# Kernel optimization log

Hardware: AMD Instinct MI355X
Metric: run time of the kernel (lower is better)

## Reference

```python
import jax, jax.numpy as jnp
import numpy as np

D_MODEL = 1024
NUM_HEAD = 16
D_HEAD = D_MODEL // NUM_HEAD
LN_EPS = 1e-5


def setup_inputs() -> dict:
    key = jax.random.key(0)
    ks = jax.random.split(key, 4)
    B, S = 4, 2048
    x = jax.random.normal(ks[0], (B, S, D_MODEL), dtype=jnp.float32)
    Wq = jax.random.normal(ks[1], (D_MODEL, D_MODEL), dtype=jnp.float32) * 0.02
    Wk = jax.random.normal(ks[2], (D_MODEL, D_MODEL), dtype=jnp.float32) * 0.02
    Wv = jax.random.normal(ks[3], (D_MODEL, D_MODEL), dtype=jnp.float32) * 0.02
    return {
        "x": x,
        "Wq": Wq, "bq": jnp.zeros((D_MODEL,), jnp.float32),
        "Wk": Wk, "bk": jnp.zeros((D_MODEL,), jnp.float32),
        "Wv": Wv, "bv": jnp.zeros((D_MODEL,), jnp.float32),
        "gamma": jnp.ones((D_MODEL,), jnp.float32),
        "beta": jnp.zeros((D_MODEL,), jnp.float32),
    }


def _layer_norm(x, gamma, beta):
    mu = jnp.mean(x, axis=-1, keepdims=True)
    var = jnp.mean(jnp.square(x - mu), axis=-1, keepdims=True)
    return (x - mu) * jax.lax.rsqrt(var + LN_EPS) * gamma + beta


def reference(x, Wq, bq, Wk, bk, Wv, bv, gamma, beta):
    # x: (B, S, D). Prefill path (kv_cache=None); dropout is eval-mode identity.
    B, S, D = x.shape
    q = (x @ Wq + bq).reshape(B, S, NUM_HEAD, D_HEAD).transpose(0, 2, 1, 3)  # (B,H,S,dh)
    k = (x @ Wk + bk).reshape(B, S, NUM_HEAD, D_HEAD).transpose(0, 2, 1, 3)
    v = (x @ Wv + bv).reshape(B, S, NUM_HEAD, D_HEAD).transpose(0, 2, 1, 3)
    scores = jnp.einsum("bhqd,bhkd->bhqk", q, k) / jnp.sqrt(jnp.float32(D_HEAD))
    causal = jnp.tril(jnp.ones((S, S), dtype=bool))  # (S, Skv) with no cache
    scores = jnp.where(causal[None, None], scores, -jnp.inf)
    w = jax.nn.softmax(scores, axis=-1)
    attn = jnp.einsum("bhqk,bhkd->bhqd", w, v).transpose(0, 2, 1, 3).reshape(B, S, D)
    out = _layer_norm(x + attn, gamma, beta)
    return out, k, v  # (output, new K cache, new V cache)
```

## Files before the change

kernel.cpp:

```cpp
#include <hip/hip_runtime.h>
#include <math.h>

#define D_MODEL 1024
#define NUM_HEAD 16
#define D_HEAD   64
#define BATCH    4
#define SEQ      2048
#define MTOT     (BATCH*SEQ)

typedef __attribute__((ext_vector_type(8))) short short8;
typedef __attribute__((ext_vector_type(4))) short short4v;
typedef __attribute__((ext_vector_type(2))) short short2v;
typedef __attribute__((ext_vector_type(4))) float f32x4;

static __device__ __forceinline__ unsigned short f2bf_u(float f) {
    union { float f; unsigned u; } v; v.f = f;
    return (unsigned short)((v.u + 0x7FFFu + ((v.u >> 16) & 1u)) >> 16);
}
static __device__ __forceinline__ short f2bf(float f) { return (short)f2bf_u(f); }
static __device__ __forceinline__ float bf2f(unsigned short h) {
    union { float f; unsigned u; } v; v.u = ((unsigned)h) << 16; return v.f;
}

#define ASYNC16(ldst, gsrc) __builtin_amdgcn_global_load_lds( \
    (const __attribute__((address_space(1))) unsigned int*)(gsrc), \
    (__attribute__((address_space(3))) unsigned int*)(ldst), 16, 0, 0)

__global__ __launch_bounds__(256) void conv_x(
    const float* __restrict__ x, unsigned short* __restrict__ hi,
    unsigned short* __restrict__ lo, int m0)
{
    const int gid = blockIdx.x * 256 + threadIdx.x;
    const int ml = gid >> 7;
    const int k  = (gid & 127) << 3;
    const float* s = &x[(size_t)(m0 + ml) * D_MODEL + k];
    float4 a = *(const float4*)s;
    float4 b = *(const float4*)(s + 4);
    float vv[8] = {a.x, a.y, a.z, a.w, b.x, b.y, b.z, b.w};
    short8 ph, pl;
#pragma unroll
    for (int j = 0; j < 8; ++j) {
        unsigned short h = f2bf_u(vv[j]);
        ph[j] = (short)h;
        pl[j] = (short)f2bf_u(vv[j] - bf2f(h));
    }
    size_t off = ((size_t)(ml >> 7) * 32 + (k >> 5)) * 4096
               + (size_t)(ml & 127) * 32 + (k & 31);
    *(short8*)&hi[off] = ph;
    *(short8*)&lo[off] = pl;
}

__global__ __launch_bounds__(256) void conv_w(
    const float* __restrict__ W, unsigned short* __restrict__ hi,
    unsigned short* __restrict__ lo)
{
    __shared__ float Tr[32][132];
    const int t  = threadIdx.x;
    const int n0 = blockIdx.x * 128, k0 = blockIdx.y * 32;
#pragma unroll
    for (int it = 0; it < 4; ++it) {
        int idx = it * 256 + t;
        int kr = idx >> 5, c = (idx & 31) * 4;
        *(float4*)&Tr[kr][c] = *(const float4*)&W[(size_t)(k0 + kr) * D_MODEL + n0 + c];
    }
    __syncthreads();
    const int n = t >> 1, kh = (t & 1) * 16;
    short8 ph0, ph1, pl0, pl1;
#pragma unroll
    for (int j = 0; j < 16; ++j) {
        float v = Tr[kh + j][n];
        unsigned short h = f2bf_u(v);
        unsigned short lw = f2bf_u(v - bf2f(h));
        if (j < 8) { ph0[j] = (short)h; pl0[j] = (short)lw; }
        else       { ph1[j - 8] = (short)h; pl1[j - 8] = (short)lw; }
    }
    size_t base = ((size_t)blockIdx.x * 32 + blockIdx.y) * 4096 + (size_t)n * 32 + kh;
    *(short8*)&hi[base]     = ph0;
    *(short8*)&hi[base + 8] = ph1;
    *(short8*)&lo[base]     = pl0;
    *(short8*)&lo[base + 8] = pl1;
}

__global__ __launch_bounds__(256) void gemm3(
    const unsigned short* __restrict__ Ah, const unsigned short* __restrict__ Al,
    const unsigned short* __restrict__ Bh, const unsigned short* __restrict__ Bl,
    const float* __restrict__ bias, float* __restrict__ Y, int m0)
{
    __shared__ unsigned short lds[16384];
    unsigned short* LA  = lds;
    unsigned short* LB  = lds + 4096;
    unsigned short* LAl = lds + 8192;
    unsigned short* LBl = lds + 12288;

    const int t  = threadIdx.x;
    const int l  = t & 63, w = t >> 6;
    const int lq = l & 15, g = l >> 4;
    const int wr = w >> 1, wc = w & 1;

    const size_t abase = (size_t)blockIdx.y * 32 * 4096;
    const size_t bbase = (size_t)blockIdx.x * 32 * 4096;

    f32x4 acc[4][4];
#pragma unroll
    for (int i = 0; i < 4; ++i)
#pragma unroll
        for (int j = 0; j < 4; ++j) { acc[i][j][0]=0.f; acc[i][j][1]=0.f; acc[i][j][2]=0.f; acc[i][j][3]=0.f; }

    for (int ks = 0; ks < 32; ++ks) {
        const unsigned short* ga  = Ah + abase + (size_t)ks * 4096;
        const unsigned short* gal = Al + abase + (size_t)ks * 4096;
        const unsigned short* gb  = Bh + bbase + (size_t)ks * 4096;
        const unsigned short* gbl = Bl + bbase + (size_t)ks * 4096;
        __syncthreads();
        ASYNC16(&LA [t*8],        ga  + t*8);
        ASYNC16(&LA [2048 + t*8], ga  + 2048 + t*8);
        ASYNC16(&LB [t*8],        gb  + t*8);
        ASYNC16(&LB [2048 + t*8], gb  + 2048 + t*8);
        ASYNC16(&LAl[t*8],        gal + t*8);
        ASYNC16(&LAl[2048 + t*8], gal + 2048 + t*8);
        ASYNC16(&LBl[t*8],        gbl + t*8);
        ASYNC16(&LBl[2048 + t*8], gbl + 2048 + t*8);
        __syncthreads();

        short8 ah[4], al[4];
#pragma unroll
        for (int fm = 0; fm < 4; ++fm) {
            int off = (wr*64 + fm*16 + lq) * 32 + g*8;
            ah[fm] = *(const short8*)&LA [off];
            al[fm] = *(const short8*)&LAl[off];
        }
#pragma unroll
        for (int fn = 0; fn < 4; ++fn) {
            int off = (wc*64 + fn*16 + lq) * 32 + g*8;
            short8 bh = *(const short8*)&LB [off];
            short8 bl = *(const short8*)&LBl[off];
#pragma unroll
            for (int fm = 0; fm < 4; ++fm) {
                acc[fm][fn] = __builtin_amdgcn_mfma_f32_16x16x32_bf16(ah[fm], bh, acc[fm][fn], 0, 0, 0);
                acc[fm][fn] = __builtin_amdgcn_mfma_f32_16x16x32_bf16(al[fm], bh, acc[fm][fn], 0, 0, 0);
                acc[fm][fn] = __builtin_amdgcn_mfma_f32_16x16x32_bf16(ah[fm], bl, acc[fm][fn], 0, 0, 0);
            }
        }
    }

    const int nb = blockIdx.x*128 + wc*64;
#pragma unroll
    for (int fn = 0; fn < 4; ++fn) {
        int n = nb + fn*16 + lq;
        int h = n >> 6, dl = n & 63;
        float bv = bias[n];
#pragma unroll
        for (int fm = 0; fm < 4; ++fm) {
            int mg = m0 + blockIdx.y*128 + wr*64 + fm*16 + g*4;
#pragma unroll
            for (int r = 0; r < 4; ++r) {
                int m  = mg + r;
                int bi = m >> 11, sr = m & (SEQ - 1);
                Y[(((size_t)bi*NUM_HEAD + h)*SEQ + sr)*D_HEAD + dl] = acc[fm][fn][r] + bv;
            }
        }
    }
}

__global__ __launch_bounds__(512) void attn_mfma(
    const float* __restrict__ Q, const float* __restrict__ K,
    const float* __restrict__ V, float* __restrict__ O)
{
    __shared__ char smem[32*1024];
    const int t  = threadIdx.x;
    const int w  = t >> 6;
    const int l  = t & 63;
    const int lq = l & 15;
    const int g  = l >> 4;

    const int bh = blockIdx.y;
    const int q0 = blockIdx.x * 128;
    const float* Qb = Q + (size_t)bh * SEQ * D_HEAD;
    const float* Kb = K + (size_t)bh * SEQ * D_HEAD;
    const float* Vb = V + (size_t)bh * SEQ * D_HEAD;

    const int qrow = q0 + w*16 + lq;

    short8 qf[2];
    {
        const float* qp = &Qb[(size_t)qrow * D_HEAD];
#pragma unroll
        for (int c = 0; c < 2; ++c) {
            float4 x0 = *(const float4*)&qp[c*32 + g*8];
            float4 x1 = *(const float4*)&qp[c*32 + g*8 + 4];
            short8 f;
            f[0]=f2bf(x0.x*0.125f); f[1]=f2bf(x0.y*0.125f);
            f[2]=f2bf(x0.z*0.125f); f[3]=f2bf(x0.w*0.125f);
            f[4]=f2bf(x1.x*0.125f); f[5]=f2bf(x1.y*0.125f);
            f[6]=f2bf(x1.z*0.125f); f[7]=f2bf(x1.w*0.125f);
            qf[c] = f;
        }
    }

    f32x4 o[4];
#pragma unroll
    for (int i = 0; i < 4; ++i) { o[i][0]=0.f; o[i][1]=0.f; o[i][2]=0.f; o[i][3]=0.f; }
    float m = -INFINITY, lsum = 0.f;

    const int pbase = 16384 + w*2048;
    const int dd  = (t & 15) * 4;
    const int rot = (t >> 1) & 3;

    for (int kvb = 0; kvb <= q0 + 64; kvb += 64) {
        __syncthreads();
#pragma unroll
        for (int u = 0; u < 2; ++u) {
            int kv = (t >> 4) + 32*u;
            float4 x = *(const float4*)&Kb[(size_t)(kvb + kv) * D_HEAD + dd];
            short4v pk; pk[0]=f2bf(x.x); pk[1]=f2bf(x.y); pk[2]=f2bf(x.z); pk[3]=f2bf(x.w);
            *(short4v*)(smem + kv*128 + ((dd*2) ^ ((kv & 7) << 4))) = pk;
        }
        {
            int p2 = t >> 4;
            float4 a = *(const float4*)&Vb[(size_t)(kvb + 2*p2    ) * D_HEAD + dd];
            float4 b = *(const float4*)&Vb[(size_t)(kvb + 2*p2 + 1) * D_HEAD + dd];
            float av[4] = {a.x, a.y, a.z, a.w};
            float bv[4] = {b.x, b.y, b.z, b.w};
#pragma unroll
            for (int j = 0; j < 4; ++j) {
                int jp  = (j + rot) & 3;
                int row = dd + jp;
                short2v pk; pk[0] = f2bf(av[jp]); pk[1] = f2bf(bv[jp]);
                *(short2v*)(smem + 8192 + row*128 + ((p2*4) ^ ((row & 7) << 4))) = pk;
            }
        }
        __syncthreads();

        f32x4 st[4];
#pragma unroll
        for (int tt = 0; tt < 4; ++tt) {
            int row = tt*16 + lq;
            const char* base = smem + row*128;
            short8 ka0 = *(const short8*)(base + ((     16*g) ^ ((row & 7) << 4)));
            short8 ka1 = *(const short8*)(base + ((64 + 16*g) ^ ((row & 7) << 4)));
            f32x4 z; z[0]=0.f; z[1]=0.f; z[2]=0.f; z[3]=0.f;
            z = __builtin_amdgcn_mfma_f32_16x16x32_bf16(ka0, qf[0], z, 0, 0, 0);
            z = __builtin_amdgcn_mfma_f32_16x16x32_bf16(ka1, qf[1], z, 0, 0, 0);
            st[tt] = z;
        }

        float tmax = -INFINITY;
#pragma unroll
        for (int tt = 0; tt < 4; ++tt)
#pragma unroll
            for (int r = 0; r < 4; ++r) {
                int kv = kvb + tt*16 + g*4 + r;
                float s = (kv <= qrow) ? st[tt][r] : -INFINITY;
                st[tt][r] = s;
                tmax = fmaxf(tmax, s);
            }
        tmax = fmaxf(tmax, __shfl_xor(tmax, 16));
        tmax = fmaxf(tmax, __shfl_xor(tmax, 32));

        float mnew = fmaxf(m, tmax);
        float scl  = __expf(m - mnew);
        m = mnew;
        lsum *= scl;
        float sr0 = __shfl(scl, 20*g + 0);
        float sr1 = __shfl(scl, 20*g + 1);
        float sr2 = __shfl(scl, 20*g + 2);
        float sr3 = __shfl(scl, 20*g + 3);
#pragma unroll
        for (int dc = 0; dc < 4; ++dc) {
            o[dc][0] *= sr0; o[dc][1] *= sr1; o[dc][2] *= sr2; o[dc][3] *= sr3;
        }

#pragma unroll
        for (int tt = 0; tt < 4; ++tt) {
            float p0 = __expf(st[tt][0] - mnew);
            float p1 = __expf(st[tt][1] - mnew);
            float p2f= __expf(st[tt][2] - mnew);
            float p3 = __expf(st[tt][3] - mnew);
            lsum += (p0 + p1) + (p2f + p3);
            short4v pk; pk[0]=f2bf(p0); pk[1]=f2bf(p1); pk[2]=f2bf(p2f); pk[3]=f2bf(p3);
            *(short4v*)(smem + pbase + lq*128 + ((32*tt + 8*g) ^ ((lq & 7) << 4))) = pk;
        }

        short8 pa0 = *(const short8*)(smem + pbase + lq*128 + ((     16*g) ^ ((lq & 7) << 4)));
        short8 pa1 = *(const short8*)(smem + pbase + lq*128 + ((64 + 16*g) ^ ((lq & 7) << 4)));
#pragma unroll
        for (int dc = 0; dc < 4; ++dc) {
            int row = dc*16 + lq;
            const char* vb = smem + 8192 + row*128;
            short8 v0 = *(const short8*)(vb + ((     16*g) ^ ((row & 7) << 4)));
            short8 v1 = *(const short8*)(vb + ((64 + 16*g) ^ ((row & 7) << 4)));
            o[dc] = __builtin_amdgcn_mfma_f32_16x16x32_bf16(pa0, v0, o[dc], 0, 0, 0);
            o[dc] = __builtin_amdgcn_mfma_f32_16x16x32_bf16(pa1, v1, o[dc], 0, 0, 0);
        }
    }

    lsum += __shfl_xor(lsum, 16);
    lsum += __shfl_xor(lsum, 32);
    float linv = 1.f / lsum;
    float lr0 = __shfl(linv, 20*g + 0);
    float lr1 = __shfl(linv, 20*g + 1);
    float lr2 = __shfl(linv, 20*g + 2);
    float lr3 = __shfl(linv, 20*g + 3);

    const int b = bh >> 4, h = bh & 15;
    float* Ob = O + ((size_t)b * SEQ + q0 + w*16) * D_MODEL + h * D_HEAD;
#pragma unroll
    for (int dc = 0; dc < 4; ++dc) {
        int col = dc*16 + lq;
        Ob[(4*g + 0)*D_MODEL + col] = o[dc][0] * lr0;
        Ob[(4*g + 1)*D_MODEL + col] = o[dc][1] * lr1;
        Ob[(4*g + 2)*D_MODEL + col] = o[dc][2] * lr2;
        Ob[(4*g + 3)*D_MODEL + col] = o[dc][3] * lr3;
    }
}

__global__ __launch_bounds__(256) void resid_ln(
    const float* __restrict__ X, const float* __restrict__ A,
    const float* __restrict__ gamma, const float* __restrict__ beta,
    float* __restrict__ Out)
{
    const int rowi = blockIdx.x;
    const size_t base = (size_t)rowi * D_MODEL;
    const int t = threadIdx.x;
    const int c = t * 4;

    float4 xv = *(const float4*)&X[base + c];
    float4 av = *(const float4*)&A[base + c];
    float v0 = xv.x + av.x, v1 = xv.y + av.y, v2 = xv.z + av.z, v3 = xv.w + av.w;

    float s1 = v0 + v1 + v2 + v3;
    float s2 = v0*v0 + v1*v1 + v2*v2 + v3*v3;

#pragma unroll
    for (int off = 32; off > 0; off >>= 1) {
        s1 += __shfl_down(s1, off);
        s2 += __shfl_down(s2, off);
    }

    __shared__ float r1[4], r2[4];
    __shared__ float mu_s, rstd_s;
    const int wid = t >> 6, lane = t & 63;
    if (lane == 0) { r1[wid] = s1; r2[wid] = s2; }
    __syncthreads();
    if (t == 0) {
        float S1 = r1[0]+r1[1]+r1[2]+r1[3];
        float S2 = r2[0]+r2[1]+r2[2]+r2[3];
        float mu  = S1 * (1.f/1024.f);
        float var = S2 * (1.f/1024.f) - mu*mu;
        mu_s   = mu;
        rstd_s = rsqrtf(var + 1e-5f);
    }
    __syncthreads();
    const float mu = mu_s, rstd = rstd_s;

    float4 gq = *(const float4*)&gamma[c];
    float4 be = *(const float4*)&beta[c];
    float4 ov = make_float4((v0-mu)*rstd*gq.x + be.x,
                            (v1-mu)*rstd*gq.y + be.y,
                            (v2-mu)*rstd*gq.z + be.z,
                            (v3-mu)*rstd*gq.w + be.w);
    *(float4*)&Out[base + c] = ov;
}

extern "C" void kernel_launch(void* const* d_in, const int* in_sizes, int n_in,
                              void* d_out, int out_size, void* d_ws, size_t ws_size,
                              hipStream_t stream)
{
    (void)in_sizes; (void)n_in; (void)out_size;

    const float* x     = (const float*)d_in[0];
    const float* Wq    = (const float*)d_in[1];
    const float* bq    = (const float*)d_in[2];
    const float* Wk    = (const float*)d_in[3];
    const float* bk    = (const float*)d_in[4];
    const float* Wv    = (const float*)d_in[5];
    const float* bv    = (const float*)d_in[6];
    const float* gamma = (const float*)d_in[7];
    const float* beta  = (const float*)d_in[8];

    float* out  = (float*)d_out;
    float* kout = out  + (size_t)MTOT * D_MODEL;
    float* vout = kout + (size_t)MTOT * D_MODEL;
    float* qtmp = out;
    float* attn = (float*)d_ws;

    const size_t W_ELT  = (size_t)D_MODEL * D_MODEL;
    const size_t need_full = (size_t)MTOT*D_MODEL*2*2 + 6*W_ELT*2;
    const int nh = (ws_size >= need_full) ? 1 : 2;
    const int HM = MTOT / nh;

    unsigned short* xh  = (unsigned short*)d_ws;
    unsigned short* xl  = xh + (size_t)HM * D_MODEL;
    unsigned short* wp  = xl + (size_t)HM * D_MODEL;
    unsigned short* wqh = wp;             unsigned short* wql = wqh + W_ELT;
    unsigned short* wkh = wql + W_ELT;    unsigned short* wkl = wkh + W_ELT;
    unsigned short* wvh = wkl + W_ELT;    unsigned short* wvl = wvh + W_ELT;

    conv_w<<<dim3(8, 32), 256, 0, stream>>>(Wq, wqh, wql);
    conv_w<<<dim3(8, 32), 256, 0, stream>>>(Wk, wkh, wkl);
    conv_w<<<dim3(8, 32), 256, 0, stream>>>(Wv, wvh, wvl);

    for (int hh = 0; hh < nh; ++hh) {
        const int m0 = hh * HM;
        conv_x<<<HM / 2, 256, 0, stream>>>(x, xh, xl, m0);
        dim3 gg(8, HM / 128);
        gemm3<<<gg, 256, 0, stream>>>(xh, xl, wqh, wql, bq, qtmp, m0);
        gemm3<<<gg, 256, 0, stream>>>(xh, xl, wkh, wkl, bk, kout, m0);
        gemm3<<<gg, 256, 0, stream>>>(xh, xl, wvh, wvl, bv, vout, m0);
    }

    attn_mfma<<<dim3(SEQ / 128, BATCH * NUM_HEAD), 512, 0, stream>>>(qtmp, kout, vout, attn);

    resid_ln<<<MTOT, 256, 0, stream>>>(x, attn, gamma, beta, out);
}
```

Baseline: 472.5 us.

## Pre-pack K and transposed V to bf16 and stream via async LDS loads

Adds a pack_kv kernel that converts K to bf16 and writes V transposed in bf16. A new attention kernel then double-buffers K/V tiles into swizzled LDS with global_load_lds, uses packed bf16 conversion, and passes P through LDS for the PV MFMA. The aim is to halve K/V read traffic, remove in-loop fp32-to-bf16 conversion, and overlap loads with compute. The cost is an extra pass over K/V and workspace usage at fixed offsets (32MB/48MB). The new path is taken only when the workspace is at least 64MB, and in that case it also forces the single-pass GEMM.

```diff
diff --git a/kernel.cpp b/kernel.cpp
--- a/kernel.cpp
+++ b/kernel.cpp
@@ -20,6 +20,11 @@
 static __device__ __forceinline__ short f2bf(float f) { return (short)f2bf_u(f); }
 static __device__ __forceinline__ float bf2f(unsigned short h) {
     union { float f; unsigned u; } v; v.u = ((unsigned)h) << 16; return v.f;
+}
+static __device__ __forceinline__ unsigned cvt_pk_bf16(float a, float b) {
+    unsigned r;
+    asm volatile("v_cvt_pk_bf16_f32 %0, %1, %2" : "=v"(r) : "v"(a), "v"(b));
+    return r;
 }
 
 #define ASYNC16(ldst, gsrc) __builtin_amdgcn_global_load_lds( \
@@ -162,6 +167,217 @@
     }
 }
 
+__global__ __launch_bounds__(256) void pack_kv(
+    const float* __restrict__ Kf, const float* __restrict__ Vf,
+    unsigned short* __restrict__ Kb, unsigned short* __restrict__ VTb)
+{
+    __shared__ float vt[64][65];
+    const int bh = blockIdx.y;
+    const int s0 = blockIdx.x * 64;
+    const int t  = threadIdx.x;
+    const int r  = t >> 2;
+    const int c  = (t & 3) * 16;
+
+    {
+        const float* ks = Kf + ((size_t)bh*SEQ + s0 + r) * D_HEAD + c;
+        float4 f0 = ((const float4*)ks)[0], f1 = ((const float4*)ks)[1];
+        float4 f2 = ((const float4*)ks)[2], f3 = ((const float4*)ks)[3];
+        float v0[8] = {f0.x,f0.y,f0.z,f0.w,f1.x,f1.y,f1.z,f1.w};
+        float v1[8] = {f2.x,f2.y,f2.z,f2.w,f3.x,f3.y,f3.z,f3.w};
+        short8 o0, o1;
+#pragma unroll
+        for (int j = 0; j < 8; ++j) { o0[j] = f2bf(v0[j]); o1[j] = f2bf(v1[j]); }
+        unsigned short* kd = Kb + ((size_t)bh*SEQ + s0 + r) * D_HEAD + c;
+        *(short8*)kd = o0; *(short8*)(kd + 8) = o1;
+    }
+
+    {
+        const float* vs = Vf + ((size_t)bh*SEQ + s0 + r) * D_HEAD + c;
+        float4 f0 = ((const float4*)vs)[0], f1 = ((const float4*)vs)[1];
+        float4 f2 = ((const float4*)vs)[2], f3 = ((const float4*)vs)[3];
+        float vv[16] = {f0.x,f0.y,f0.z,f0.w,f1.x,f1.y,f1.z,f1.w,
+                        f2.x,f2.y,f2.z,f2.w,f3.x,f3.y,f3.z,f3.w};
+#pragma unroll
+        for (int j = 0; j < 16; ++j) vt[r][c + j] = vv[j];
+    }
+    __syncthreads();
+    {
+        const int d  = t >> 2;
+        const int kv = (t & 3) * 16;
+        short8 o0, o1;
+#pragma unroll
+        for (int j = 0; j < 8; ++j)  o0[j] = f2bf(vt[kv + j][d]);
+#pragma unroll
+        for (int j = 0; j < 8; ++j)  o1[j] = f2bf(vt[kv + 8 + j][d]);
+        unsigned short* vd = VTb + ((size_t)bh*D_HEAD + d) * SEQ + s0 + kv;
+        *(short8*)vd = o0; *(short8*)(vd + 8) = o1;
+    }
+}
+
+__global__ __launch_bounds__(512) void attn_mfma2(
+    const float* __restrict__ Q, const unsigned short* __restrict__ Kbf,
+    const unsigned short* __restrict__ VT, float* __restrict__ O)
+{
+    __shared__ __attribute__((aligned(16))) char smem[48*1024];
+    const int t  = threadIdx.x;
+    const int w  = t >> 6;
+    const int l  = t & 63;
+    const int lq = l & 15;
+    const int g  = l >> 4;
+
+    const int bh = blockIdx.y;
+    const int q0 = blockIdx.x * 128;
+    const float* Qb = Q + (size_t)bh * SEQ * D_HEAD;
+    const char*  Kb = (const char*)(Kbf + (size_t)bh * SEQ * D_HEAD);
+    const char*  Vb = (const char*)(VT  + (size_t)bh * D_HEAD * SEQ);
+
+    const int qrow = q0 + w*16 + lq;
+
+    short8 qf[2];
+    {
+        const float* qp = &Qb[(size_t)qrow * D_HEAD];
+#pragma unroll
+        for (int c = 0; c < 2; ++c) {
+            float4 x0 = *(const float4*)&qp[c*32 + g*8];
+            float4 x1 = *(const float4*)&qp[c*32 + g*8 + 4];
+            union { unsigned u[4]; short8 s8; } pk;
+            pk.u[0] = cvt_pk_bf16(x0.x*0.125f, x0.y*0.125f);
+            pk.u[1] = cvt_pk_bf16(x0.z*0.125f, x0.w*0.125f);
+            pk.u[2] = cvt_pk_bf16(x1.x*0.125f, x1.y*0.125f);
+            pk.u[3] = cvt_pk_bf16(x1.z*0.125f, x1.w*0.125f);
+            qf[c] = pk.s8;
+        }
+    }
+
+    f32x4 o[4];
+#pragma unroll
+    for (int i = 0; i < 4; ++i) { o[i][0]=0.f; o[i][1]=0.f; o[i][2]=0.f; o[i][3]=0.f; }
+    float m = -INFINITY, lsum = 0.f;
+
+    const int pbase = 32768 + w*2048;
+
+    const int srow  = t >> 3;
+    const int sbyte = ((t & 7) * 16) ^ ((srow & 7) << 4);
+    const int ldst  = t * 16;
+
+#define STAGE(bufi, kv0) do {                                                   \
+    ASYNC16(smem + (bufi)*8192 + ldst,                                          \
+            Kb + (size_t)((kv0) + srow) * 128 + sbyte);                         \
+    ASYNC16(smem + 16384 + (bufi)*8192 + ldst,                                  \
+            Vb + (size_t)srow * (SEQ*2) + (size_t)(kv0) * 2 + sbyte);           \
+} while (0)
+
+    const int nt = (q0 >> 6) + 2;
+    STAGE(0, 0);
+
+    for (int ti = 0; ti < nt; ++ti) {
+        const int cur = ti & 1;
+        const int kvb = ti * 64;
+        if (ti + 1 < nt) {
+            STAGE(cur ^ 1, kvb + 64);
+            asm volatile("s_waitcnt vmcnt(2)" ::: "memory");
+        } else {
+            asm volatile("s_waitcnt vmcnt(0)" ::: "memory");
+        }
+        __builtin_amdgcn_s_barrier();
+        __builtin_amdgcn_sched_barrier(0);
+
+        const char* kbase = smem + cur*8192;
+        const char* vbase = smem + 16384 + cur*8192;
+
+        f32x4 st[4];
+        __builtin_amdgcn_s_setprio(1);
+#pragma unroll
+        for (int tt = 0; tt < 4; ++tt) {
+            int row = tt*16 + lq;
+            const char* base = kbase + row*128;
+            short8 ka0 = *(const short8*)(base + ((     16*g) ^ ((row & 7) << 4)));
+            short8 ka1 = *(const short8*)(base + ((64 + 16*g) ^ ((row & 7) << 4)));
+            f32x4 z; z[0]=0.f; z[1]=0.f; z[2]=0.f; z[3]=0.f;
+            z = __builtin_amdgcn_mfma_f32_16x16x32_bf16(ka0, qf[0], z, 0, 0, 0);
+            z = __builtin_amdgcn_mfma_f32_16x16x32_bf16(ka1, qf[1], z, 0, 0, 0);
+            st[tt] = z;
+        }
+        __builtin_amdgcn_s_setprio(0);
+
+        float tmax = -INFINITY;
+#pragma unroll
+        for (int tt = 0; tt < 4; ++tt)
+#pragma unroll
+            for (int r = 0; r < 4; ++r) {
+                int kv = kvb + tt*16 + g*4 + r;
+                float s = (kv <= qrow) ? st[tt][r] : -INFINITY;
+                st[tt][r] = s;
+                tmax = fmaxf(tmax, s);
+            }
+        tmax = fmaxf(tmax, __shfl_xor(tmax, 16));
+        tmax = fmaxf(tmax, __shfl_xor(tmax, 32));
+
+        float mnew = fmaxf(m, tmax);
+        float scl  = __expf(m - mnew);
+        m = mnew;
+        lsum *= scl;
+        float sr0 = __shfl(scl, 20*g + 0);
+        float sr1 = __shfl(scl, 20*g + 1);
+        float sr2 = __shfl(scl, 20*g + 2);
+        float sr3 = __shfl(scl, 20*g + 3);
+#pragma unroll
+        for (int dc = 0; dc < 4; ++dc) {
+            o[dc][0] *= sr0; o[dc][1] *= sr1; o[dc][2] *= sr2; o[dc][3] *= sr3;
+        }
+
+#pragma unroll
+        for (int tt = 0; tt < 4; ++tt) {
+            float p0 = __expf(st[tt][0] - mnew);
+            float p1 = __expf(st[tt][1] - mnew);
+            float p2f= __expf(st[tt][2] - mnew);
+            float p3 = __expf(st[tt][3] - mnew);
+            lsum += (p0 + p1) + (p2f + p3);
+            uint2 pw;
+            pw.x = cvt_pk_bf16(p0, p1);
+            pw.y = cvt_pk_bf16(p2f, p3);
+            *(uint2*)(smem + pbase + lq*128 + ((32*tt + 8*g) ^ ((lq & 7) << 4))) = pw;
+        }
+
+        short8 pa0 = *(const short8*)(smem + pbase + lq*128 + ((     16*g) ^ ((lq & 7) << 4)));
+        short8 pa1 = *(const short8*)(smem + pbase + lq*128 + ((64 + 16*g) ^ ((lq & 7) << 4)));
+        __builtin_amdgcn_s_setprio(1);
+#pragma unroll
+        for (int dc = 0; dc < 4; ++dc) {
+            int row = dc*16 + lq;
+            const char* vb = vbase + row*128;
+            short8 v0 = *(const short8*)(vb + ((     16*g) ^ ((row & 7) << 4)));
+            short8 v1 = *(const short8*)(vb + ((64 + 16*g) ^ ((row & 7) << 4)));
+            o[dc] = __builtin_amdgcn_mfma_f32_16x16x32_bf16(pa0, v0, o[dc], 0, 0, 0);
+            o[dc] = __builtin_amdgcn_mfma_f32_16x16x32_bf16(pa1, v1, o[dc], 0, 0, 0);
+        }
+        __builtin_amdgcn_s_setprio(0);
+
+        __builtin_amdgcn_sched_barrier(0);
+        __builtin_amdgcn_s_barrier();
+    }
+#undef STAGE
+
+    lsum += __shfl_xor(lsum, 16);
+    lsum += __shfl_xor(lsum, 32);
+    float linv = 1.f / lsum;
+    float lr0 = __shfl(linv, 20*g + 0);
+    float lr1 = __shfl(linv, 20*g + 1);
+    float lr2 = __shfl(linv, 20*g + 2);
+    float lr3 = __shfl(linv, 20*g + 3);
+
+    const int b = bh >> 4, h = bh & 15;
+    float* Ob = O + ((size_t)b * SEQ + q0 + w*16) * D_MODEL + h * D_HEAD;
+#pragma unroll
+    for (int dc = 0; dc < 4; ++dc) {
+        int col = dc*16 + lq;
+        Ob[(4*g + 0)*D_MODEL + col] = o[dc][0] * lr0;
+        Ob[(4*g + 1)*D_MODEL + col] = o[dc][1] * lr1;
+        Ob[(4*g + 2)*D_MODEL + col] = o[dc][2] * lr2;
+        Ob[(4*g + 3)*D_MODEL + col] = o[dc][3] * lr3;
+    }
+}
+
 __global__ __launch_bounds__(512) void attn_mfma(
     const float* __restrict__ Q, const float* __restrict__ K,
     const float* __restrict__ V, float* __restrict__ O)
@@ -384,9 +600,11 @@
     float* qtmp = out;
     float* attn = (float*)d_ws;
 
-    const size_t W_ELT  = (size_t)D_MODEL * D_MODEL;
+    const size_t MB = 1024*1024;
+    const size_t W_ELT = (size_t)D_MODEL * D_MODEL;
     const size_t need_full = (size_t)MTOT*D_MODEL*2*2 + 6*W_ELT*2;
-    const int nh = (ws_size >= need_full) ? 1 : 2;
+    const bool newpath = (ws_size >= 64*MB);
+    const int nh = (newpath || ws_size >= need_full) ? 1 : 2;
     const int HM = MTOT / nh;
 
     unsigned short* xh  = (unsigned short*)d_ws;
@@ -409,7 +627,14 @@
         gemm3<<<gg, 256, 0, stream>>>(xh, xl, wvh, wvl, bv, vout, m0);
     }
 
-    attn_mfma<<<dim3(SEQ / 128, BATCH * NUM_HEAD), 512, 0, stream>>>(qtmp, kout, vout, attn);
+    if (newpath) {
+        unsigned short* gKbf = (unsigned short*)((char*)d_ws + 32*MB);
+        unsigned short* gVT  = (unsigned short*)((char*)d_ws + 48*MB);
+        pack_kv<<<dim3(SEQ/64, BATCH*NUM_HEAD), 256, 0, stream>>>(kout, vout, gKbf, gVT);
+        attn_mfma2<<<dim3(SEQ/128, BATCH*NUM_HEAD), 512, 0, stream>>>(qtmp, gKbf, gVT, attn);
+    } else {
+        attn_mfma<<<dim3(SEQ/128, BATCH*NUM_HEAD), 512, 0, stream>>>(qtmp, kout, vout, attn);
+    }
 
     resid_ln<<<MTOT, 256, 0, stream>>>(x, attn, gamma, beta, out);
 }
```

New measurement: 448.2 us. 5.1% less time.

## Drop weight low-part in projections, prepack K/V bf16 and double-buffer attention loads

Applied to the files above, without the earlier changes.

The projection GEMMs now split only x into hi/lo bf16 and keep weights as a single bf16 part, which cuts one of three MFMAs and a quarter of the LDS traffic per step. A new pack_kv kernel converts K to bf16 and transposes V to bf16 once, so the attention kernel can stream K/V tiles with asynchronous global-to-LDS loads into a double buffer. The attention kernel also reverses block order so the longest causal rows start first, and uses packed bf16 conversion and s_setprio around the MFMAs. The trade-off is lower accuracy in the projections, since the weight residual is dropped, and an extra pass plus a fixed workspace layout that assumes enough memory.

```diff
diff --git a/kernel.cpp b/kernel.cpp
--- a/kernel.cpp
+++ b/kernel.cpp
@@ -20,6 +20,11 @@
 static __device__ __forceinline__ short f2bf(float f) { return (short)f2bf_u(f); }
 static __device__ __forceinline__ float bf2f(unsigned short h) {
     union { float f; unsigned u; } v; v.u = ((unsigned)h) << 16; return v.f;
+}
+static __device__ __forceinline__ unsigned cvt_pk_bf16(float a, float b) {
+    unsigned r;
+    asm volatile("v_cvt_pk_bf16_f32 %0, %1, %2" : "=v"(r) : "v"(a), "v"(b));
+    return r;
 }
 
 #define ASYNC16(ldst, gsrc) __builtin_amdgcn_global_load_lds( \
@@ -51,8 +56,7 @@
 }
 
 __global__ __launch_bounds__(256) void conv_w(
-    const float* __restrict__ W, unsigned short* __restrict__ hi,
-    unsigned short* __restrict__ lo)
+    const float* __restrict__ W, unsigned short* __restrict__ hi)
 {
     __shared__ float Tr[32][132];
     const int t  = threadIdx.x;
@@ -65,32 +69,26 @@
     }
     __syncthreads();
     const int n = t >> 1, kh = (t & 1) * 16;
-    short8 ph0, ph1, pl0, pl1;
+    short8 ph0, ph1;
 #pragma unroll
     for (int j = 0; j < 16; ++j) {
-        float v = Tr[kh + j][n];
-        unsigned short h = f2bf_u(v);
-        unsigned short lw = f2bf_u(v - bf2f(h));
-        if (j < 8) { ph0[j] = (short)h; pl0[j] = (short)lw; }
-        else       { ph1[j - 8] = (short)h; pl1[j - 8] = (short)lw; }
+        unsigned short h = f2bf_u(Tr[kh + j][n]);
+        if (j < 8) ph0[j] = (short)h; else ph1[j - 8] = (short)h;
     }
     size_t base = ((size_t)blockIdx.x * 32 + blockIdx.y) * 4096 + (size_t)n * 32 + kh;
     *(short8*)&hi[base]     = ph0;
     *(short8*)&hi[base + 8] = ph1;
-    *(short8*)&lo[base]     = pl0;
-    *(short8*)&lo[base + 8] = pl1;
 }
 
 __global__ __launch_bounds__(256) void gemm3(
     const unsigned short* __restrict__ Ah, const unsigned short* __restrict__ Al,
-    const unsigned short* __restrict__ Bh, const unsigned short* __restrict__ Bl,
+    const unsigned short* __restrict__ Bh,
     const float* __restrict__ bias, float* __restrict__ Y, int m0)
 {
-    __shared__ unsigned short lds[16384];
+    __shared__ unsigned short lds[12288];
     unsigned short* LA  = lds;
     unsigned short* LB  = lds + 4096;
     unsigned short* LAl = lds + 8192;
-    unsigned short* LBl = lds + 12288;
 
     const int t  = threadIdx.x;
     const int l  = t & 63, w = t >> 6;
@@ -110,7 +108,6 @@
         const unsigned short* ga  = Ah + abase + (size_t)ks * 4096;
         const unsigned short* gal = Al + abase + (size_t)ks * 4096;
         const unsigned short* gb  = Bh + bbase + (size_t)ks * 4096;
-        const unsigned short* gbl = Bl + bbase + (size_t)ks * 4096;
         __syncthreads();
         ASYNC16(&LA [t*8],        ga  + t*8);
         ASYNC16(&LA [2048 + t*8], ga  + 2048 + t*8);
@@ -118,8 +115,6 @@
         ASYNC16(&LB [2048 + t*8], gb  + 2048 + t*8);
         ASYNC16(&LAl[t*8],        gal + t*8);
         ASYNC16(&LAl[2048 + t*8], gal + 2048 + t*8);
-        ASYNC16(&LBl[t*8],        gbl + t*8);
-        ASYNC16(&LBl[2048 + t*8], gbl + 2048 + t*8);
         __syncthreads();
 
         short8 ah[4], al[4];
@@ -132,13 +127,11 @@
 #pragma unroll
         for (int fn = 0; fn < 4; ++fn) {
             int off = (wc*64 + fn*16 + lq) * 32 + g*8;
-            short8 bh = *(const short8*)&LB [off];
-            short8 bl = *(const short8*)&LBl[off];
+            short8 bh = *(const short8*)&LB[off];
 #pragma unroll
             for (int fm = 0; fm < 4; ++fm) {
                 acc[fm][fn] = __builtin_amdgcn_mfma_f32_16x16x32_bf16(ah[fm], bh, acc[fm][fn], 0, 0, 0);
                 acc[fm][fn] = __builtin_amdgcn_mfma_f32_16x16x32_bf16(al[fm], bh, acc[fm][fn], 0, 0, 0);
-                acc[fm][fn] = __builtin_amdgcn_mfma_f32_16x16x32_bf16(ah[fm], bl, acc[fm][fn], 0, 0, 0);
             }
         }
     }
@@ -162,11 +155,58 @@
     }
 }
 
-__global__ __launch_bounds__(512) void attn_mfma(
-    const float* __restrict__ Q, const float* __restrict__ K,
-    const float* __restrict__ V, float* __restrict__ O)
-{
-    __shared__ char smem[32*1024];
+__global__ __launch_bounds__(256) void pack_kv(
+    const float* __restrict__ Kf, const float* __restrict__ Vf,
+    unsigned short* __restrict__ Kb, unsigned short* __restrict__ VTb)
+{
+    __shared__ float vt[64][65];
+    const int bh = blockIdx.y;
+    const int s0 = blockIdx.x * 64;
+    const int t  = threadIdx.x;
+    const int r  = t >> 2;
+    const int c  = (t & 3) * 16;
+
+    {
+        const float* ks = Kf + ((size_t)bh*SEQ + s0 + r) * D_HEAD + c;
+        float4 f0 = ((const float4*)ks)[0], f1 = ((const float4*)ks)[1];
+        float4 f2 = ((const float4*)ks)[2], f3 = ((const float4*)ks)[3];
+        float v0[8] = {f0.x,f0.y,f0.z,f0.w,f1.x,f1.y,f1.z,f1.w};
+        float v1[8] = {f2.x,f2.y,f2.z,f2.w,f3.x,f3.y,f3.z,f3.w};
+        short8 o0, o1;
+#pragma unroll
+        for (int j = 0; j < 8; ++j) { o0[j] = f2bf(v0[j]); o1[j] = f2bf(v1[j]); }
+        unsigned short* kd = Kb + ((size_t)bh*SEQ + s0 + r) * D_HEAD + c;
+        *(short8*)kd = o0; *(short8*)(kd + 8) = o1;
+    }
+
+    {
+        const float* vs = Vf + ((size_t)bh*SEQ + s0 + r) * D_HEAD + c;
+        float4 f0 = ((const float4*)vs)[0], f1 = ((const float4*)vs)[1];
+        float4 f2 = ((const float4*)vs)[2], f3 = ((const float4*)vs)[3];
+        float vv[16] = {f0.x,f0.y,f0.z,f0.w,f1.x,f1.y,f1.z,f1.w,
+                        f2.x,f2.y,f2.z,f2.w,f3.x,f3.y,f3.z,f3.w};
+#pragma unroll
+        for (int j = 0; j < 16; ++j) vt[r][c + j] = vv[j];
+    }
+    __syncthreads();
+    {
+        const int d  = t >> 2;
+        const int kv = (t & 3) * 16;
+        short8 o0, o1;
+#pragma unroll
+        for (int j = 0; j < 8; ++j)  o0[j] = f2bf(vt[kv + j][d]);
+#pragma unroll
+        for (int j = 0; j < 8; ++j)  o1[j] = f2bf(vt[kv + 8 + j][d]);
+        unsigned short* vd = VTb + ((size_t)bh*D_HEAD + d) * SEQ + s0 + kv;
+        *(short8*)vd = o0; *(short8*)(vd + 8) = o1;
+    }
+}
+
+__global__ __launch_bounds__(512) void attn_mfma2(
+    const float* __restrict__ Q, const unsigned short* __restrict__ Kbf,
+    const unsigned short* __restrict__ VT, float* __restrict__ O)
+{
+    __shared__ __attribute__((aligned(16))) char smem[48*1024];
     const int t  = threadIdx.x;
     const int w  = t >> 6;
     const int l  = t & 63;
@@ -174,10 +214,10 @@
     const int g  = l >> 4;
 
     const int bh = blockIdx.y;
-    const int q0 = blockIdx.x * 128;
+    const int q0 = (gridDim.x - 1 - blockIdx.x) * 128;
     const float* Qb = Q + (size_t)bh * SEQ * D_HEAD;
-    const float* Kb = K + (size_t)bh * SEQ * D_HEAD;
-    const float* Vb = V + (size_t)bh * SEQ * D_HEAD;
+    const char*  Kb = (const char*)(Kbf + (size_t)bh * SEQ * D_HEAD);
+    const char*  Vb = (const char*)(VT  + (size_t)bh * D_HEAD * SEQ);
 
     const int qrow = q0 + w*16 + lq;
 
@@ -188,12 +228,12 @@
         for (int c = 0; c < 2; ++c) {
             float4 x0 = *(const float4*)&qp[c*32 + g*8];
             float4 x1 = *(const float4*)&qp[c*32 + g*8 + 4];
-            short8 f;
-            f[0]=f2bf(x0.x*0.125f); f[1]=f2bf(x0.y*0.125f);
-            f[2]=f2bf(x0.z*0.125f); f[3]=f2bf(x0.w*0.125f);
-            f[4]=f2bf(x1.x*0.125f); f[5]=f2bf(x1.y*0.125f);
-            f[6]=f2bf(x1.z*0.125f); f[7]=f2bf(x1.w*0.125f);
-            qf[c] = f;
+            union { unsigned u[4]; short8 s8; } pk;
+            pk.u[0] = cvt_pk_bf16(x0.x*0.125f, x0.y*0.125f);
+            pk.u[1] = cvt_pk_bf16(x0.z*0.125f, x0.w*0.125f);
+            pk.u[2] = cvt_pk_bf16(x1.x*0.125f, x1.y*0.125f);
+            pk.u[3] = cvt_pk_bf16(x1.z*0.125f, x1.w*0.125f);
+            qf[c] = pk.s8;
         }
     }
 
@@ -202,40 +242,43 @@
     for (int i = 0; i < 4; ++i) { o[i][0]=0.f; o[i][1]=0.f; o[i][2]=0.f; o[i][3]=0.f; }
     float m = -INFINITY, lsum = 0.f;
 
-    const int pbase = 16384 + w*2048;
-    const int dd  = (t & 15) * 4;
-    const int rot = (t >> 1) & 3;
-
-    for (int kvb = 0; kvb <= q0 + 64; kvb += 64) {
-        __syncthreads();
-#pragma unroll
-        for (int u = 0; u < 2; ++u) {
-            int kv = (t >> 4) + 32*u;
-            float4 x = *(const float4*)&Kb[(size_t)(kvb + kv) * D_HEAD + dd];
-            short4v pk; pk[0]=f2bf(x.x); pk[1]=f2bf(x.y); pk[2]=f2bf(x.z); pk[3]=f2bf(x.w);
-            *(short4v*)(smem + kv*128 + ((dd*2) ^ ((kv & 7) << 4))) = pk;
-        }
-        {
-            int p2 = t >> 4;
-            float4 a = *(const float4*)&Vb[(size_t)(kvb + 2*p2    ) * D_HEAD + dd];
-            float4 b = *(const float4*)&Vb[(size_t)(kvb + 2*p2 + 1) * D_HEAD + dd];
-            float av[4] = {a.x, a.y, a.z, a.w};
-            float bv[4] = {b.x, b.y, b.z, b.w};
-#pragma unroll
-            for (int j = 0; j < 4; ++j) {
-                int jp  = (j + rot) & 3;
-                int row = dd + jp;
-                short2v pk; pk[0] = f2bf(av[jp]); pk[1] = f2bf(bv[jp]);
-                *(short2v*)(smem + 8192 + row*128 + ((p2*4) ^ ((row & 7) << 4))) = pk;
-            }
-        }
-        __syncthreads();
+    const int pbase = 32768 + w*2048;
+
+    const int srow  = t >> 3;
+    const int sbyte = ((t & 7) * 16) ^ ((srow & 7) << 4);
+    const int ldst  = t * 16;
+
+#define STAGE(bufi, kv0) do {                                                   \
+    ASYNC16(smem + (bufi)*8192 + ldst,                                          \
+            Kb + (size_t)((kv0) + srow) * 128 + sbyte);                         \
+    ASYNC16(smem + 16384 + (bufi)*8192 + ldst,                                  \
+            Vb + (size_t)srow * (SEQ*2) + (size_t)(kv0) * 2 + sbyte);           \
+} while (0)
+
+    const int nt = (q0 >> 6) + 2;
+    STAGE(0, 0);
+
+    for (int ti = 0; ti < nt; ++ti) {
+        const int cur = ti & 1;
+        const int kvb = ti * 64;
+        if (ti + 1 < nt) {
+            STAGE(cur ^ 1, kvb + 64);
+            asm volatile("s_waitcnt vmcnt(2)" ::: "memory");
+        } else {
+            asm volatile("s_waitcnt vmcnt(0)" ::: "memory");
+        }
+        __builtin_amdgcn_s_barrier();
+        __builtin_amdgcn_sched_barrier(0);
+
+        const char* kbase = smem + cur*8192;
+        const char* vbase = smem + 16384 + cur*8192;
 
         f32x4 st[4];
+        __builtin_amdgcn_s_setprio(1);
 #pragma unroll
         for (int tt = 0; tt < 4; ++tt) {
             int row = tt*16 + lq;
-            const char* base = smem + row*128;
+            const char* base = kbase + row*128;
             short8 ka0 = *(const short8*)(base + ((     16*g) ^ ((row & 7) << 4)));
             short8 ka1 = *(const short8*)(base + ((64 + 16*g) ^ ((row & 7) << 4)));
             f32x4 z; z[0]=0.f; z[1]=0.f; z[2]=0.f; z[3]=0.f;
@@ -243,6 +286,7 @@
             z = __builtin_amdgcn_mfma_f32_16x16x32_bf16(ka1, qf[1], z, 0, 0, 0);
             st[tt] = z;
         }
+        __builtin_amdgcn_s_setprio(0);
 
         float tmax = -INFINITY;
 #pragma unroll
@@ -277,22 +321,30 @@
             float p2f= __expf(st[tt][2] - mnew);
             float p3 = __expf(st[tt][3] - mnew);
             lsum += (p0 + p1) + (p2f + p3);
-            short4v pk; pk[0]=f2bf(p0); pk[1]=f2bf(p1); pk[2]=f2bf(p2f); pk[3]=f2bf(p3);
-            *(short4v*)(smem + pbase + lq*128 + ((32*tt + 8*g) ^ ((lq & 7) << 4))) = pk;
+            uint2 pw;
+            pw.x = cvt_pk_bf16(p0, p1);
+            pw.y = cvt_pk_bf16(p2f, p3);
+            *(uint2*)(smem + pbase + lq*128 + ((32*tt + 8*g) ^ ((lq & 7) << 4))) = pw;
         }
 
         short8 pa0 = *(const short8*)(smem + pbase + lq*128 + ((     16*g) ^ ((lq & 7) << 4)));
         short8 pa1 = *(const short8*)(smem + pbase + lq*128 + ((64 + 16*g) ^ ((lq & 7) << 4)));
+        __builtin_amdgcn_s_setprio(1);
 #pragma unroll
         for (int dc = 0; dc < 4; ++dc) {
             int row = dc*16 + lq;
-            const char* vb = smem + 8192 + row*128;
+            const char* vb = vbase + row*128;
             short8 v0 = *(const short8*)(vb + ((     16*g) ^ ((row & 7) << 4)));
             short8 v1 = *(const short8*)(vb + ((64 + 16*g) ^ ((row & 7) << 4)));
             o[dc] = __builtin_amdgcn_mfma_f32_16x16x32_bf16(pa0, v0, o[dc], 0, 0, 0);
             o[dc] = __builtin_amdgcn_mfma_f32_16x16x32_bf16(pa1, v1, o[dc], 0, 0, 0);
         }
-    }
+        __builtin_amdgcn_s_setprio(0);
+
+        __builtin_amdgcn_sched_barrier(0);
+        __builtin_amdgcn_s_barrier();
+    }
+#undef STAGE
 
     lsum += __shfl_xor(lsum, 16);
     lsum += __shfl_xor(lsum, 32);
@@ -366,7 +418,7 @@
                               void* d_out, int out_size, void* d_ws, size_t ws_size,
                               hipStream_t stream)
 {
-    (void)in_sizes; (void)n_in; (void)out_size;
+    (void)in_sizes; (void)n_in; (void)out_size; (void)ws_size;
 
     const float* x     = (const float*)d_in[0];
     const float* Wq    = (const float*)d_in[1];
@@ -384,32 +436,29 @@
     float* qtmp = out;
     float* attn = (float*)d_ws;
 
-    const size_t W_ELT  = (size_t)D_MODEL * D_MODEL;
-    const size_t need_full = (size_t)MTOT*D_MODEL*2*2 + 6*W_ELT*2;
-    const int nh = (ws_size >= need_full) ? 1 : 2;
-    const int HM = MTOT / nh;
+    const size_t MB = 1024*1024;
+    const size_t W_ELT = (size_t)D_MODEL * D_MODEL;
 
     unsigned short* xh  = (unsigned short*)d_ws;
-    unsigned short* xl  = xh + (size_t)HM * D_MODEL;
-    unsigned short* wp  = xl + (size_t)HM * D_MODEL;
-    unsigned short* wqh = wp;             unsigned short* wql = wqh + W_ELT;
-    unsigned short* wkh = wql + W_ELT;    unsigned short* wkl = wkh + W_ELT;
-    unsigned short* wvh = wkl + W_ELT;    unsigned short* wvl = wvh + W_ELT;
-
-    conv_w<<<dim3(8, 32), 256, 0, stream>>>(Wq, wqh, wql);
-    conv_w<<<dim3(8, 32), 256, 0, stream>>>(Wk, wkh, wkl);
-    conv_w<<<dim3(8, 32), 256, 0, stream>>>(Wv, wvh, wvl);
-
-    for (int hh = 0; hh < nh; ++hh) {
-        const int m0 = hh * HM;
-        conv_x<<<HM / 2, 256, 0, stream>>>(x, xh, xl, m0);
-        dim3 gg(8, HM / 128);
-        gemm3<<<gg, 256, 0, stream>>>(xh, xl, wqh, wql, bq, qtmp, m0);
-        gemm3<<<gg, 256, 0, stream>>>(xh, xl, wkh, wkl, bk, kout, m0);
-        gemm3<<<gg, 256, 0, stream>>>(xh, xl, wvh, wvl, bv, vout, m0);
-    }
-
-    attn_mfma<<<dim3(SEQ / 128, BATCH * NUM_HEAD), 512, 0, stream>>>(qtmp, kout, vout, attn);
+    unsigned short* xl  = xh + (size_t)MTOT * D_MODEL;
+    unsigned short* wqh = (unsigned short*)((char*)d_ws + 32*MB);
+    unsigned short* wkh = wqh + W_ELT;
+    unsigned short* wvh = wkh + W_ELT;
+
+    conv_w<<<dim3(8, 32), 256, 0, stream>>>(Wq, wqh);
+    conv_w<<<dim3(8, 32), 256, 0, stream>>>(Wk, wkh);
+    conv_w<<<dim3(8, 32), 256, 0, stream>>>(Wv, wvh);
+
+    conv_x<<<MTOT / 2, 256, 0, stream>>>(x, xh, xl, 0);
+    dim3 gg(8, MTOT / 128);
+    gemm3<<<gg, 256, 0, stream>>>(xh, xl, wqh, bq, qtmp, 0);
+    gemm3<<<gg, 256, 0, stream>>>(xh, xl, wkh, bk, kout, 0);
+    gemm3<<<gg, 256, 0, stream>>>(xh, xl, wvh, bv, vout, 0);
+
+    unsigned short* gKbf = (unsigned short*)((char*)d_ws + 32*MB);
+    unsigned short* gVT  = (unsigned short*)((char*)d_ws + 48*MB);
+    pack_kv<<<dim3(SEQ/64, BATCH*NUM_HEAD), 256, 0, stream>>>(kout, vout, gKbf, gVT);
+    attn_mfma2<<<dim3(SEQ/128, BATCH*NUM_HEAD), 512, 0, stream>>>(qtmp, gKbf, gVT, attn);
 
     resid_ln<<<MTOT, 256, 0, stream>>>(x, attn, gamma, beta, out);
 }
```

Measured after the change: 422.1 us. 1.12x faster.
